# Performance work log

Measured on AMD Instinct MI355X. Metric: run time of the kernel, lower is better.

## Reference

```python
import jax, jax.numpy as jnp
import numpy as np

RANK = 16
SHAPE = (512, 512, 512)


def setup_inputs() -> dict:
    key = jax.random.key(0)
    k0, k1, k2 = jax.random.split(key, 3)
    # factors initialized like torch.randn(rank, n_dim) / 100.0
    f0 = jax.random.normal(k0, (RANK, SHAPE[0]), dtype=jnp.float32) / 100.0
    f1 = jax.random.normal(k1, (RANK, SHAPE[1]), dtype=jnp.float32) / 100.0
    f2 = jax.random.normal(k2, (RANK, SHAPE[2]), dtype=jnp.float32) / 100.0
    return {"f0": f0, "f1": f1, "f2": f2}


def reference(f0, f1, f2):
    # CP/PARAFAC reconstruction: sum over rank of outer products.
    # Equivalent to torch.einsum('ka,kb,kc->abc', f0, f1, f2).
    # Expressed so XLA contracts (ka,kb->abk) via GEMM then (abk,kc->abc):
    return jnp.einsum('ka,kb,kc->abc', f0, f1, f2)
```

## Files before the change

### kernel.cpp

```cpp
#include <hip/hip_runtime.h>

#define RANK 16
#define N 512

typedef float vfloat4 __attribute__((ext_vector_type(4)));

__global__ __launch_bounds__(256) void parafac_kernel(
    const float* __restrict__ f0,
    const float* __restrict__ f1,
    const float* __restrict__ f2,
    float* __restrict__ out)
{
    __shared__ float pt[RANK][N];

    const int t    = threadIdx.x;
    const int wave = t >> 6;
    const int lane = t & 63;
    const int a    = blockIdx.x;

    {
        const int sk   = t >> 4;
        const int sbi0 = (t & 15) * 4;
        const float s  = f0[sk * N + a];
#pragma unroll
        for (int j = 0; j < 8; ++j) {
            const int sbi = sbi0 + j * 64;
            const vfloat4 f1v = *reinterpret_cast<const vfloat4*>(&f1[sk * N + sbi]);
            *reinterpret_cast<vfloat4*>(&pt[sk][sbi]) = s * f1v;
        }
    }

    const int c4 = (wave & 1) * 256 + lane * 4;
    vfloat4 v[RANK];
#pragma unroll
    for (int k = 0; k < RANK; ++k)
        v[k] = *reinterpret_cast<const vfloat4*>(&f2[k * N + c4]);

    __syncthreads();

    const int bhalf = (wave >> 1) * 256;
    float* outa = out + (size_t)a * N * N + c4;

#pragma unroll 2
    for (int it = 0; it < 64; ++it) {
        const int bb = bhalf + it * 4;
        vfloat4 acc0 = (vfloat4)(0.f);
        vfloat4 acc1 = (vfloat4)(0.f);
        vfloat4 acc2 = (vfloat4)(0.f);
        vfloat4 acc3 = (vfloat4)(0.f);
#pragma unroll
        for (int k = 0; k < RANK; ++k) {
            const vfloat4 pk = *reinterpret_cast<const vfloat4*>(&pt[k][bb]);
            const vfloat4 vk = v[k];
            acc0 += pk.x * vk;
            acc1 += pk.y * vk;
            acc2 += pk.z * vk;
            acc3 += pk.w * vk;
        }
        float* o = outa + (size_t)bb * N;
        *reinterpret_cast<vfloat4*>(o)         = acc0;
        *reinterpret_cast<vfloat4*>(o + N)     = acc1;
        *reinterpret_cast<vfloat4*>(o + 2 * N) = acc2;
        *reinterpret_cast<vfloat4*>(o + 3 * N) = acc3;
    }
}

extern "C" void kernel_launch(void* const* d_in, const int* in_sizes, int n_in,
                              void* d_out, int out_size, void* d_ws, size_t ws_size,
                              hipStream_t stream) {
    const float* f0 = (const float*)d_in[0];
    const float* f1 = (const float*)d_in[1];
    const float* f2 = (const float*)d_in[2];
    float* out = (float*)d_out;

    dim3 grid(N);
    dim3 block(256);
    parafac_kernel<<<grid, block, 0, stream>>>(f0, f1, f2, out);
}
```

Baseline: 116.1 us.

## Split each a-slice across two blocks and transpose shared product tile

The grid doubles so each block handles half of the b rows for one a, and the shared product table becomes row-major [b][k]. Each wave reads one row's 16 products as broadcast vector loads and writes a single output row per iteration instead of four. The aim is more blocks in flight and a cheaper shared-memory access pattern. In exchange, f2 register loads and setup are repeated across twice as many blocks, and the scalar, uncoalesced-style pt fill costs more per block.

```diff
diff --git a/kernel.cpp b/kernel.cpp
--- a/kernel.cpp
+++ b/kernel.cpp
@@ -2,6 +2,7 @@
 
 #define RANK 16
 #define N 512
+#define ROWS 256
 
 typedef float vfloat4 __attribute__((ext_vector_type(4)));
 
@@ -11,23 +12,20 @@
     const float* __restrict__ f2,
     float* __restrict__ out)
 {
-    __shared__ float pt[RANK][N];
+    __shared__ float pt[ROWS][RANK];
 
     const int t    = threadIdx.x;
     const int wave = t >> 6;
     const int lane = t & 63;
-    const int a    = blockIdx.x;
+    const int blk  = blockIdx.x;
+    const int a    = blk >> 1;
+    const int bb0  = (blk & 1) * ROWS;
 
     {
-        const int sk   = t >> 4;
-        const int sbi0 = (t & 15) * 4;
-        const float s  = f0[sk * N + a];
+        const int b = bb0 + t;
 #pragma unroll
-        for (int j = 0; j < 8; ++j) {
-            const int sbi = sbi0 + j * 64;
-            const vfloat4 f1v = *reinterpret_cast<const vfloat4*>(&f1[sk * N + sbi]);
-            *reinterpret_cast<vfloat4*>(&pt[sk][sbi]) = s * f1v;
-        }
+        for (int k = 0; k < RANK; ++k)
+            pt[t][k] = f0[k * N + a] * f1[k * N + b];
     }
 
     const int c4 = (wave & 1) * 256 + lane * 4;
@@ -38,30 +36,26 @@
 
     __syncthreads();
 
-    const int bhalf = (wave >> 1) * 256;
-    float* outa = out + (size_t)a * N * N + c4;
+    const int rofs = wave >> 1;
+    float* outb = out + ((size_t)a * N + bb0) * N + c4;
 
 #pragma unroll 2
-    for (int it = 0; it < 64; ++it) {
-        const int bb = bhalf + it * 4;
-        vfloat4 acc0 = (vfloat4)(0.f);
-        vfloat4 acc1 = (vfloat4)(0.f);
-        vfloat4 acc2 = (vfloat4)(0.f);
-        vfloat4 acc3 = (vfloat4)(0.f);
+    for (int it = 0; it < ROWS / 2; ++it) {
+        const int r = it * 2 + rofs;
+        vfloat4 p0 = *reinterpret_cast<const vfloat4*>(&pt[r][0]);
+        vfloat4 p1 = *reinterpret_cast<const vfloat4*>(&pt[r][4]);
+        vfloat4 p2 = *reinterpret_cast<const vfloat4*>(&pt[r][8]);
+        vfloat4 p3 = *reinterpret_cast<const vfloat4*>(&pt[r][12]);
+
+        vfloat4 acc = (vfloat4)(0.f);
 #pragma unroll
-        for (int k = 0; k < RANK; ++k) {
-            const vfloat4 pk = *reinterpret_cast<const vfloat4*>(&pt[k][bb]);
-            const vfloat4 vk = v[k];
-            acc0 += pk.x * vk;
-            acc1 += pk.y * vk;
-            acc2 += pk.z * vk;
-            acc3 += pk.w * vk;
+        for (int j = 0; j < 4; ++j) {
+            acc += p0[j] * v[j];
+            acc += p1[j] * v[4 + j];
+            acc += p2[j] * v[8 + j];
+            acc += p3[j] * v[12 + j];
         }
-        float* o = outa + (size_t)bb * N;
-        *reinterpret_cast<vfloat4*>(o)         = acc0;
-        *reinterpret_cast<vfloat4*>(o + N)     = acc1;
-        *reinterpret_cast<vfloat4*>(o + 2 * N) = acc2;
-        *reinterpret_cast<vfloat4*>(o + 3 * N) = acc3;
+        *reinterpret_cast<vfloat4*>(outb + (size_t)r * N) = acc;
     }
 }
 
@@ -73,7 +67,7 @@
     const float* f2 = (const float*)d_in[2];
     float* out = (float*)d_out;
 
-    dim3 grid(N);
+    dim3 grid(N * 2);
     dim3 block(256);
     parafac_kernel<<<grid, block, 0, stream>>>(f0, f1, f2, out);
 }
```

Result: faster. 106.9 us (-7.9%).
